# Performance work log

Hardware: AMD Instinct MI355X
Metric: run time of the kernel (lower is better)

The kernel has to match this reference:

```python
import jax, jax.numpy as jnp
import numpy as np

R = 32          # voxel resolution (init kwarg)
EPS = 0.0       # init kwarg eps


def _norm_coords(coords):
    # coords: [B, 3, N]
    nc = coords - coords.mean(axis=2, keepdims=True)
    # L2 norm over xyz (dim=1), max over points (dim=2)
    denom = jnp.linalg.norm(nc, axis=1, keepdims=True).max(axis=2, keepdims=True) * 2.0 + EPS
    nc = nc / denom + 0.5
    return jnp.clip(nc * R, 0.0, R - 1)  # [B, 3, N] in [0, R-1]


def setup_inputs() -> dict:
    key = jax.random.key(0)
    k1, k2 = jax.random.split(key)
    features = jax.random.normal(k1, (8, 64, 65536), dtype=jnp.float32)
    coords = jax.random.normal(k2, (8, 3, 65536), dtype=jnp.float32)
    return {"features": features, "coords": coords}


def reference(features, coords):
    # features: [B, C, N], coords: [B, 3, N]
    nc = _norm_coords(coords)
    vox = jnp.round(nc).astype(jnp.int32)                      # [B, 3, N]
    flat = (vox[:, 0] * R + vox[:, 1]) * R + vox[:, 2]         # [B, N] flat voxel ids

    def per_batch(f, idx):
        # f: [C, N], idx: [N] -> scatter-mean into R^3 voxels
        sums = jax.ops.segment_sum(f.T, idx, num_segments=R ** 3)            # [R^3, C]
        cnt = jax.ops.segment_sum(jnp.ones(idx.shape, jnp.float32), idx,
                                  num_segments=R ** 3)                        # [R^3]
        return (sums / jnp.maximum(cnt, 1.0)[:, None]).T                      # [C, R^3]

    vox_feat = jax.vmap(per_batch)(features, flat)             # [B, C, R^3]
    B, C = features.shape[0], features.shape[1]
    return vox_feat.reshape(B, C, R, R, R), nc
```

## Files before the change

kernel.cpp:

```cpp
#include <hip/hip_runtime.h>
#include <hip/hip_fp16.h>

#define RR 32
#define R3 32768
#define NPTS 65536
#define NCH 64
#define NB 8


__global__ void mean1_kernel(const float* __restrict__ coords, double* __restrict__ part) {
    __shared__ double ls[3][4];
    int b = blockIdx.y, blk = blockIdx.x;
    int t = threadIdx.x;
    const float* cb = coords + (size_t)b * 3 * NPTS;
    int base = blk * 1024 + t;
    double sx = 0.0, sy = 0.0, sz = 0.0;
#pragma unroll
    for (int k = 0; k < 4; k++) {
        int n = base + k * 256;
        sx += cb[n];
        sy += cb[NPTS + n];
        sz += cb[2 * NPTS + n];
    }
    for (int off = 32; off > 0; off >>= 1) {
        sx += __shfl_down(sx, off);
        sy += __shfl_down(sy, off);
        sz += __shfl_down(sz, off);
    }
    int wave = t >> 6;
    if ((t & 63) == 0) { ls[0][wave] = sx; ls[1][wave] = sy; ls[2][wave] = sz; }
    __syncthreads();
    if (t == 0) {
        part[((size_t)b * 64 + blk) * 3 + 0] = ls[0][0] + ls[0][1] + ls[0][2] + ls[0][3];
        part[((size_t)b * 64 + blk) * 3 + 1] = ls[1][0] + ls[1][1] + ls[1][2] + ls[1][3];
        part[((size_t)b * 64 + blk) * 3 + 2] = ls[2][0] + ls[2][1] + ls[2][2] + ls[2][3];
    }
}

__global__ void mean2_kernel(const double* __restrict__ part, float* __restrict__ meanf) {
    int b = blockIdx.x, l = threadIdx.x;
    double sx = part[((size_t)b * 64 + l) * 3 + 0];
    double sy = part[((size_t)b * 64 + l) * 3 + 1];
    double sz = part[((size_t)b * 64 + l) * 3 + 2];
    for (int off = 32; off > 0; off >>= 1) {
        sx += __shfl_down(sx, off);
        sy += __shfl_down(sy, off);
        sz += __shfl_down(sz, off);
    }
    if (l == 0) {
        meanf[b * 4 + 0] = (float)(sx * (1.0 / NPTS));
        meanf[b * 4 + 1] = (float)(sy * (1.0 / NPTS));
        meanf[b * 4 + 2] = (float)(sz * (1.0 / NPTS));
    }
}

__global__ void max1_kernel(const float* __restrict__ coords,
                            const float* __restrict__ meanf,
                            float* __restrict__ partmax) {
    __shared__ float ls[4];
    int b = blockIdx.y, blk = blockIdx.x;
    int t = threadIdx.x;
    float mx = meanf[b * 4 + 0], my = meanf[b * 4 + 1], mz = meanf[b * 4 + 2];
    const float* cb = coords + (size_t)b * 3 * NPTS;
    int base = blk * 1024 + t;
    float m = 0.0f;
#pragma unroll
    for (int k = 0; k < 4; k++) {
        int n = base + k * 256;
        float dx = cb[n] - mx;
        float dy = cb[NPTS + n] - my;
        float dz = cb[2 * NPTS + n] - mz;
        m = fmaxf(m, dx * dx + dy * dy + dz * dz);
    }
    for (int off = 32; off > 0; off >>= 1) m = fmaxf(m, __shfl_down(m, off));
    int wave = t >> 6;
    if ((t & 63) == 0) ls[wave] = m;
    __syncthreads();
    if (t == 0) partmax[b * 64 + blk] = fmaxf(fmaxf(ls[0], ls[1]), fmaxf(ls[2], ls[3]));
}

__global__ void max2_kernel(const float* __restrict__ partmax, float* __restrict__ denom) {
    int b = blockIdx.x, l = threadIdx.x;
    float m = partmax[b * 64 + l];
    for (int off = 32; off > 0; off >>= 1) m = fmaxf(m, __shfl_down(m, off));
    if (l == 0) denom[b] = 2.0f * sqrtf(m);
}


__global__ void nc_vid_kernel(const float* __restrict__ coords,
                              const float* __restrict__ meanf,
                              const float* __restrict__ denomv,
                              float* __restrict__ ncout,
                              int* __restrict__ vid,
                              unsigned* __restrict__ cnt) {
    int b = blockIdx.y;
    int n = blockIdx.x * blockDim.x + threadIdx.x;
    float mx = meanf[b * 4 + 0], my = meanf[b * 4 + 1], mz = meanf[b * 4 + 2];
    float denom = denomv[b];
    const float* cb = coords + (size_t)b * 3 * NPTS;
    float dx = cb[n] - mx;
    float dy = cb[NPTS + n] - my;
    float dz = cb[2 * NPTS + n] - mz;
    float qx = fminf(fmaxf((dx / denom + 0.5f) * 32.0f, 0.0f), 31.0f);
    float qy = fminf(fmaxf((dy / denom + 0.5f) * 32.0f, 0.0f), 31.0f);
    float qz = fminf(fmaxf((dz / denom + 0.5f) * 32.0f, 0.0f), 31.0f);
    float* nb_ = ncout + (size_t)b * 3 * NPTS;
    nb_[n] = qx;
    nb_[NPTS + n] = qy;
    nb_[2 * NPTS + n] = qz;
    int flat = ((int)rintf(qx) * RR + (int)rintf(qy)) * RR + (int)rintf(qz);
    vid[b * NPTS + n] = flat;
    atomicAdd(&cnt[b * R3 + flat], 1u);
}

__global__ __launch_bounds__(1024) void scan_kernel(const unsigned* __restrict__ cnt,
                                                    unsigned* __restrict__ cursor) {
    __shared__ unsigned buf[R3 + R3 / 32];
    __shared__ unsigned ls[1024];
    int b = blockIdx.x;
    int t = threadIdx.x;
    const unsigned* c = cnt + b * R3;
    for (int i = t; i < R3; i += 1024) buf[i + (i >> 5)] = c[i];
    __syncthreads();
    int sb = t * 33;
    unsigned v[32];
    unsigned s = 0;
#pragma unroll
    for (int k = 0; k < 32; k++) {
        unsigned x = buf[sb + k];
        v[k] = s;
        s += x;
    }
    ls[t] = s;
    __syncthreads();
    for (int d = 1; d < 1024; d <<= 1) {
        unsigned x = (t >= d) ? ls[t - d] : 0u;
        __syncthreads();
        ls[t] += x;
        __syncthreads();
    }
    unsigned chunk_excl = (t == 0) ? 0u : ls[t - 1];
#pragma unroll
    for (int k = 0; k < 32; k++) buf[sb + k] = chunk_excl + v[k];
    __syncthreads();
    unsigned* cur = cursor + b * R3;
    for (int i = t; i < R3; i += 1024) cur[i] = buf[i + (i >> 5)];
}

__global__ void permute_kernel(const float* __restrict__ feats,
                               const int* __restrict__ vid,
                               unsigned* __restrict__ cursor,
                               __half* __restrict__ ft,
                               int* __restrict__ vid_sorted) {
    __shared__ float tile[64][65];
    __shared__ int spos[64];
    int b  = blockIdx.y;
    int n0 = blockIdx.x * 64;
    int t  = threadIdx.x;

    if (t < 64) {
        int flat = vid[b * NPTS + n0 + t];
        int pos = (int)atomicAdd(&cursor[b * R3 + flat], 1u);
        spos[t] = pos;
        vid_sorted[b * NPTS + pos] = flat;
    }

    const float* fb = feats + (size_t)b * NCH * NPTS + n0;
    int i  = t & 63;
    int c0w = t >> 6;
#pragma unroll
    for (int iter = 0; iter < 16; iter++) {
        int c = iter * 4 + c0w;
        tile[i][c] = fb[(size_t)c * NPTS + i];
    }
    __syncthreads();

    int wave = t >> 6;
    int lane = t & 63;
    int hp = lane >> 5;
    int c0 = (lane & 31) * 2;
    __half* fbase = ft + (size_t)b * NPTS * NCH;
#pragma unroll
    for (int j = 0; j < 8; j++) {
        int p = wave * 16 + j * 2 + hp;
        __half2 hv = __floats2half2_rn(tile[p][c0], tile[p][c0 + 1]);
        *reinterpret_cast<__half2*>(fbase + (size_t)spos[p] * NCH + c0) = hv;
    }
}

__global__ void segsum_kernel(const __half* __restrict__ ft,
                              const int* __restrict__ vid_sorted,
                              float* __restrict__ ws_vox) {
    __shared__ int sv[257];
    int b   = blockIdx.y;
    int t   = threadIdx.x;
    int bp0 = blockIdx.x * 256;

    sv[t] = vid_sorted[b * NPTS + bp0 + t];
    if (t == 0)
        sv[256] = (bp0 + 256 < NPTS) ? vid_sorted[b * NPTS + bp0 + 256] : -1;
    __syncthreads();

    int wave  = t >> 6;
    int lane  = t & 63;
    int chunk = wave * 2 + (lane >> 5);
    int c0    = (lane & 31) * 2;
    int p0    = chunk * 32;

    const __half* fb = ft + ((size_t)b * NPTS + bp0 + p0) * NCH + c0;
    float* wv = ws_vox + (size_t)b * R3 * NCH + c0;

    float sx = 0.0f, sy = 0.0f;
    int vcur = sv[p0];
#pragma unroll
    for (int k = 0; k < 32; k++) {
        __half2 h = *reinterpret_cast<const __half2*>(fb + (size_t)k * NCH);
        float2 f = __half22float2(h);
        sx += f.x;
        sy += f.y;
        int vnext = sv[p0 + k + 1];
        if (vnext != vcur) {
            atomicAdd(wv + (size_t)vcur * NCH, sx);
            atomicAdd(wv + (size_t)vcur * NCH + 1, sy);
            sx = 0.0f;
            sy = 0.0f;
            vcur = vnext;
        }
    }
    if (sx != 0.0f || sy != 0.0f) {
        atomicAdd(wv + (size_t)vcur * NCH, sx);
        atomicAdd(wv + (size_t)vcur * NCH + 1, sy);
    }
}

__global__ void normalize_t_kernel(const float* __restrict__ ws_vox,
                                   const unsigned* __restrict__ cnt,
                                   float* __restrict__ voxout) {
    __shared__ float tile[64][65];
    __shared__ float cinv[64];
    __shared__ unsigned scnt[64];
    int b  = blockIdx.y;
    int v0 = blockIdx.x * 64;
    int t  = threadIdx.x;
    if (t < 64) {
        unsigned c = cnt[b * R3 + v0 + t];
        scnt[t] = c;
        cinv[t] = 1.0f / fmaxf((float)c, 1.0f);
    }
    __syncthreads();
    const float* src = ws_vox + ((size_t)b * R3 + v0) * NCH;
    int c = t & 63;
    int w = t >> 6;
#pragma unroll
    for (int iter = 0; iter < 16; iter++) {
        int vi = iter * 4 + w;
        tile[c][vi] = scnt[vi] ? src[(size_t)vi * NCH + c] * cinv[vi] : 0.0f;
    }
    __syncthreads();
    float* dst = voxout + (size_t)b * NCH * R3 + v0;
    int vi = t & 63;
#pragma unroll
    for (int iter = 0; iter < 16; iter++) {
        int cc = iter * 4 + w;
        dst[(size_t)cc * R3 + vi] = tile[cc][vi];
    }
}


__global__ void scatter_vm_kernel(const float* __restrict__ feats,
                                  const float* __restrict__ coords,
                                  const float* __restrict__ meanf,
                                  const float* __restrict__ denomv,
                                  float* __restrict__ ws_vox,
                                  float* __restrict__ ncout,
                                  float* __restrict__ cnt) {
    __shared__ float tile[64][65];
    __shared__ int   sflat[64];
    int b  = blockIdx.y;
    int n0 = blockIdx.x * 64;
    int t  = threadIdx.x;
    if (t < 64) {
        int n = n0 + t;
        float mx = meanf[b * 4 + 0], my = meanf[b * 4 + 1], mz = meanf[b * 4 + 2];
        float denom = denomv[b];
        const float* cb = coords + (size_t)b * 3 * NPTS;
        float dx = cb[n] - mx;
        float dy = cb[NPTS + n] - my;
        float dz = cb[2 * NPTS + n] - mz;
        float qx = fminf(fmaxf((dx / denom + 0.5f) * 32.0f, 0.0f), 31.0f);
        float qy = fminf(fmaxf((dy / denom + 0.5f) * 32.0f, 0.0f), 31.0f);
        float qz = fminf(fmaxf((dz / denom + 0.5f) * 32.0f, 0.0f), 31.0f);
        float* nb_ = ncout + (size_t)b * 3 * NPTS;
        nb_[n] = qx;
        nb_[NPTS + n] = qy;
        nb_[2 * NPTS + n] = qz;
        int flat = ((int)rintf(qx) * RR + (int)rintf(qy)) * RR + (int)rintf(qz);
        sflat[t] = flat;
        atomicAdd(&cnt[b * R3 + flat], 1.0f);
    }
    const float* fb = feats + (size_t)b * NCH * NPTS + n0;
    int i = t & 63;
    int c0 = t >> 6;
#pragma unroll
    for (int iter = 0; iter < 16; iter++) {
        int c = iter * 4 + c0;
        tile[i][c] = fb[(size_t)c * NPTS + i];
    }
    __syncthreads();
    int wave = t >> 6;
    int lane = t & 63;
#pragma unroll
    for (int k = 0; k < 16; k++) {
        int p = wave * 16 + k;
        float v = tile[p][lane];
        size_t base = ((size_t)b * R3 + sflat[p]) * NCH;
        atomicAdd(&ws_vox[base + lane], v);
    }
}

__global__ void normalize_tf_kernel(const float* __restrict__ ws_vox,
                                    const float* __restrict__ cnt,
                                    float* __restrict__ voxout) {
    __shared__ float tile[64][65];
    __shared__ float cinv[64];
    int b  = blockIdx.y;
    int v0 = blockIdx.x * 64;
    int t  = threadIdx.x;
    if (t < 64) cinv[t] = 1.0f / fmaxf(cnt[b * R3 + v0 + t], 1.0f);
    __syncthreads();
    const float* src = ws_vox + ((size_t)b * R3 + v0) * NCH;
    int c = t & 63;
    int w = t >> 6;
#pragma unroll
    for (int iter = 0; iter < 16; iter++) {
        int vi = iter * 4 + w;
        tile[c][vi] = src[(size_t)vi * NCH + c] * cinv[vi];
    }
    __syncthreads();
    float* dst = voxout + (size_t)b * NCH * R3 + v0;
    int vi = t & 63;
#pragma unroll
    for (int iter = 0; iter < 16; iter++) {
        int cc = iter * 4 + w;
        dst[(size_t)cc * R3 + vi] = tile[cc][vi];
    }
}

extern "C" void kernel_launch(void* const* d_in, const int* in_sizes, int n_in,
                              void* d_out, int out_size, void* d_ws, size_t ws_size,
                              hipStream_t stream) {
    const float* feats  = (const float*)d_in[0];
    const float* coords = (const float*)d_in[1];
    float* out = (float*)d_out;
    float* voxout = out;
    float* ncout  = out + (size_t)NB * NCH * R3;

    double* part    = (double*)d_ws;
    float*  partmax = (float*)((char*)d_ws + 12544);
    float*  meanf   = (float*)((char*)d_ws + 14592);
    float*  denomv  = (float*)((char*)d_ws + 14720);

    const size_t off_cnt   = 16384;
    const size_t cnt_bytes = (size_t)NB * R3 * 4;
    const size_t off_vox   = off_cnt + cnt_bytes;
    const size_t vox_bytes = (size_t)NB * R3 * NCH * 4;
    const size_t off_cur   = off_vox + vox_bytes;
    const size_t off_vid   = off_cur + cnt_bytes;
    const size_t vid_bytes = (size_t)NB * NPTS * 4;
    const size_t off_vs    = off_vid + vid_bytes;
    const size_t off_ft    = off_vs + vid_bytes;
    const size_t ft_bytes  = (size_t)NB * NPTS * NCH * 2;
    const size_t need_sort = off_ft + ft_bytes;
    const size_t need_vm   = off_vox + vox_bytes;

    if (ws_size >= need_sort) {
        unsigned* cnt    = (unsigned*)((char*)d_ws + off_cnt);
        float*    ws_vox = (float*)((char*)d_ws + off_vox);
        unsigned* cursor = (unsigned*)((char*)d_ws + off_cur);
        int*      vid    = (int*)((char*)d_ws + off_vid);
        int*      vid_s  = (int*)((char*)d_ws + off_vs);
        __half*   ft     = (__half*)((char*)d_ws + off_ft);

        hipMemsetAsync((char*)d_ws + off_cnt, 0, cnt_bytes + vox_bytes, stream);

        mean1_kernel<<<dim3(64, NB), 256, 0, stream>>>(coords, part);
        mean2_kernel<<<NB, 64, 0, stream>>>(part, meanf);
        max1_kernel <<<dim3(64, NB), 256, 0, stream>>>(coords, meanf, partmax);
        max2_kernel <<<NB, 64, 0, stream>>>(partmax, denomv);
        nc_vid_kernel<<<dim3(NPTS / 256, NB), 256, 0, stream>>>(coords, meanf, denomv,
                                                                ncout, vid, cnt);
        scan_kernel  <<<NB, 1024, 0, stream>>>(cnt, cursor);
        permute_kernel<<<dim3(NPTS / 64, NB), 256, 0, stream>>>(feats, vid, cursor, ft, vid_s);
        segsum_kernel <<<dim3(NPTS / 256, NB), 256, 0, stream>>>(ft, vid_s, ws_vox);
        normalize_t_kernel<<<dim3(R3 / 64, NB), 256, 0, stream>>>(ws_vox, cnt, voxout);
    } else if (ws_size >= need_vm) {
        float* cntf   = (float*)((char*)d_ws + off_cnt);
        float* ws_vox = (float*)((char*)d_ws + off_vox);
        hipMemsetAsync((char*)d_ws + off_cnt, 0, cnt_bytes + vox_bytes, stream);
        mean1_kernel<<<dim3(64, NB), 256, 0, stream>>>(coords, part);
        mean2_kernel<<<NB, 64, 0, stream>>>(part, meanf);
        max1_kernel <<<dim3(64, NB), 256, 0, stream>>>(coords, meanf, partmax);
        max2_kernel <<<NB, 64, 0, stream>>>(partmax, denomv);
        scatter_vm_kernel<<<dim3(NPTS / 64, NB), 256, 0, stream>>>(
            feats, coords, meanf, denomv, ws_vox, ncout, cntf);
        normalize_tf_kernel<<<dim3(R3 / 64, NB), 256, 0, stream>>>(ws_vox, cntf, voxout);
    }
}
```

Before: 342.7 us.

## Split permute into linear transpose plus rank kernel, gather features in segsum

Before, the permute kernel scattered fp16 feature rows to their sorted positions. Now the features are transposed into a point-major fp16 buffer with contiguous writes, and a separate rank kernel builds a permutation index. The segment-sum kernel then gathers rows through that permutation instead of reading them contiguously. This trades scattered 128-byte writes for scattered 128-byte reads and adds one kernel launch plus a perm buffer. The ws_size threshold for the fallback branch is also changed.

```diff
diff --git a/kernel.cpp b/kernel.cpp
--- a/kernel.cpp
+++ b/kernel.cpp
@@ -147,30 +147,19 @@
     for (int i = t; i < R3; i += 1024) cur[i] = buf[i + (i >> 5)];
 }
 
-__global__ void permute_kernel(const float* __restrict__ feats,
-                               const int* __restrict__ vid,
-                               unsigned* __restrict__ cursor,
-                               __half* __restrict__ ft,
-                               int* __restrict__ vid_sorted) {
+__global__ void transpose_kernel(const float* __restrict__ feats,
+                                 __half* __restrict__ ftL) {
     __shared__ float tile[64][65];
-    __shared__ int spos[64];
     int b  = blockIdx.y;
     int n0 = blockIdx.x * 64;
     int t  = threadIdx.x;
 
-    if (t < 64) {
-        int flat = vid[b * NPTS + n0 + t];
-        int pos = (int)atomicAdd(&cursor[b * R3 + flat], 1u);
-        spos[t] = pos;
-        vid_sorted[b * NPTS + pos] = flat;
-    }
-
     const float* fb = feats + (size_t)b * NCH * NPTS + n0;
     int i  = t & 63;
-    int c0w = t >> 6;
-#pragma unroll
-    for (int iter = 0; iter < 16; iter++) {
-        int c = iter * 4 + c0w;
+    int cw = t >> 6;
+#pragma unroll
+    for (int iter = 0; iter < 16; iter++) {
+        int c = iter * 4 + cw;
         tile[i][c] = fb[(size_t)c * NPTS + i];
     }
     __syncthreads();
@@ -179,24 +168,39 @@
     int lane = t & 63;
     int hp = lane >> 5;
     int c0 = (lane & 31) * 2;
-    __half* fbase = ft + (size_t)b * NPTS * NCH;
+    __half* fbase = ftL + ((size_t)b * NPTS + n0) * NCH;
 #pragma unroll
     for (int j = 0; j < 8; j++) {
         int p = wave * 16 + j * 2 + hp;
         __half2 hv = __floats2half2_rn(tile[p][c0], tile[p][c0 + 1]);
-        *reinterpret_cast<__half2*>(fbase + (size_t)spos[p] * NCH + c0) = hv;
-    }
-}
-
-__global__ void segsum_kernel(const __half* __restrict__ ft,
+        *reinterpret_cast<__half2*>(fbase + (size_t)p * NCH + c0) = hv;
+    }
+}
+
+__global__ void rank_kernel(const int* __restrict__ vid,
+                            unsigned* __restrict__ cursor,
+                            int* __restrict__ perm,
+                            int* __restrict__ vid_sorted) {
+    int b = blockIdx.y;
+    int n = blockIdx.x * blockDim.x + threadIdx.x;
+    int flat = vid[b * NPTS + n];
+    int pos = (int)atomicAdd(&cursor[b * R3 + flat], 1u);
+    perm[b * NPTS + pos] = n;
+    vid_sorted[b * NPTS + pos] = flat;
+}
+
+__global__ void segsum_kernel(const __half* __restrict__ ftL,
+                              const int* __restrict__ perm,
                               const int* __restrict__ vid_sorted,
                               float* __restrict__ ws_vox) {
     __shared__ int sv[257];
+    __shared__ int sp[256];
     int b   = blockIdx.y;
     int t   = threadIdx.x;
     int bp0 = blockIdx.x * 256;
 
     sv[t] = vid_sorted[b * NPTS + bp0 + t];
+    sp[t] = perm[b * NPTS + bp0 + t];
     if (t == 0)
         sv[256] = (bp0 + 256 < NPTS) ? vid_sorted[b * NPTS + bp0 + 256] : -1;
     __syncthreads();
@@ -207,14 +211,15 @@
     int c0    = (lane & 31) * 2;
     int p0    = chunk * 32;
 
-    const __half* fb = ft + ((size_t)b * NPTS + bp0 + p0) * NCH + c0;
+    const __half* fb = ftL + (size_t)b * NPTS * NCH + c0;
     float* wv = ws_vox + (size_t)b * R3 * NCH + c0;
 
     float sx = 0.0f, sy = 0.0f;
     int vcur = sv[p0];
 #pragma unroll
     for (int k = 0; k < 32; k++) {
-        __half2 h = *reinterpret_cast<const __half2*>(fb + (size_t)k * NCH);
+        int n = sp[p0 + k];
+        __half2 h = *reinterpret_cast<const __half2*>(fb + (size_t)n * NCH);
         float2 f = __half22float2(h);
         sx += f.x;
         sy += f.y;
@@ -368,10 +373,11 @@
     const size_t off_vid   = off_cur + cnt_bytes;
     const size_t vid_bytes = (size_t)NB * NPTS * 4;
     const size_t off_vs    = off_vid + vid_bytes;
-    const size_t off_ft    = off_vs + vid_bytes;
+    const size_t off_perm  = off_vs + vid_bytes;
+    const size_t off_ft    = off_perm + vid_bytes;
     const size_t ft_bytes  = (size_t)NB * NPTS * NCH * 2;
     const size_t need_sort = off_ft + ft_bytes;
-    const size_t need_vm   = off_vox + vox_bytes;
+    const size_t need_vm   = off_cur;
 
     if (ws_size >= need_sort) {
         unsigned* cnt    = (unsigned*)((char*)d_ws + off_cnt);
@@ -379,7 +385,8 @@
         unsigned* cursor = (unsigned*)((char*)d_ws + off_cur);
         int*      vid    = (int*)((char*)d_ws + off_vid);
         int*      vid_s  = (int*)((char*)d_ws + off_vs);
-        __half*   ft     = (__half*)((char*)d_ws + off_ft);
+        int*      perm   = (int*)((char*)d_ws + off_perm);
+        __half*   ftL    = (__half*)((char*)d_ws + off_ft);
 
         hipMemsetAsync((char*)d_ws + off_cnt, 0, cnt_bytes + vox_bytes, stream);
 
@@ -390,8 +397,9 @@
         nc_vid_kernel<<<dim3(NPTS / 256, NB), 256, 0, stream>>>(coords, meanf, denomv,
                                                                 ncout, vid, cnt);
         scan_kernel  <<<NB, 1024, 0, stream>>>(cnt, cursor);
-        permute_kernel<<<dim3(NPTS / 64, NB), 256, 0, stream>>>(feats, vid, cursor, ft, vid_s);
-        segsum_kernel <<<dim3(NPTS / 256, NB), 256, 0, stream>>>(ft, vid_s, ws_vox);
+        transpose_kernel<<<dim3(NPTS / 64, NB), 256, 0, stream>>>(feats, ftL);
+        rank_kernel  <<<dim3(NPTS / 256, NB), 256, 0, stream>>>(vid, cursor, perm, vid_s);
+        segsum_kernel<<<dim3(NPTS / 256, NB), 256, 0, stream>>>(ftL, perm, vid_s, ws_vox);
         normalize_t_kernel<<<dim3(R3 / 64, NB), 256, 0, stream>>>(ws_vox, cnt, voxout);
     } else if (ws_size >= need_vm) {
         float* cntf   = (float*)((char*)d_ws + off_cnt);
```

Measured after the change: 370.2 us. 1.08x slower.

## Fuse segment sum and normalize into per-voxel-tile shared-memory accumulation

Applied to the files above, without the earlier changes.

Replaces the point-parallel segment-sum kernel, which did global float atomics into a large voxel workspace, and the separate normalize/transpose kernel with one voxel-tile kernel. Each block owns 64 voxels, takes their point range from the scan cursors, accumulates sorted fp16 features in LDS with shared atomics, then normalizes and writes transposed output. This removes the 64 MB voxel workspace memset, the global atomics and the round trip through that buffer. The cost is uneven work per block when occupied voxels vary in point count, and the cursor semantics (inclusive end vs. start) must match how the scan and permute kernels use them.

```diff
diff --git a/kernel.cpp b/kernel.cpp
--- a/kernel.cpp
+++ b/kernel.cpp
@@ -1,5 +1,6 @@
 #include <hip/hip_runtime.h>
 #include <hip/hip_fp16.h>
+#include <climits>
 
 #define RR 32
 #define R3 32768
@@ -188,81 +189,83 @@
     }
 }
 
-__global__ void segsum_kernel(const __half* __restrict__ ft,
+__global__ void voxsum_kernel(const __half* __restrict__ ft,
                               const int* __restrict__ vid_sorted,
-                              float* __restrict__ ws_vox) {
+                              const unsigned* __restrict__ cursor,
+                              const unsigned* __restrict__ cnt,
+                              float* __restrict__ voxout) {
+    __shared__ float acc[64 * 65];
+    __shared__ float cinv[64];
     __shared__ int sv[257];
-    int b   = blockIdx.y;
-    int t   = threadIdx.x;
-    int bp0 = blockIdx.x * 256;
-
-    sv[t] = vid_sorted[b * NPTS + bp0 + t];
-    if (t == 0)
-        sv[256] = (bp0 + 256 < NPTS) ? vid_sorted[b * NPTS + bp0 + 256] : -1;
-    __syncthreads();
-
+    int b  = blockIdx.y;
+    int v0 = blockIdx.x * 64;
+    int t  = threadIdx.x;
+
+    for (int i = t; i < 64 * 65; i += 256) acc[i] = 0.0f;
+    if (t < 64) cinv[t] = 1.0f / fmaxf((float)cnt[b * R3 + v0 + t], 1.0f);
+
+    unsigned start = (v0 == 0) ? 0u : cursor[b * R3 + v0 - 1];
+    unsigned end   = cursor[b * R3 + v0 + 63];
+    __syncthreads();
+
+    const int* vs = vid_sorted + (size_t)b * NPTS;
     int wave  = t >> 6;
     int lane  = t & 63;
     int chunk = wave * 2 + (lane >> 5);
     int c0    = (lane & 31) * 2;
     int p0    = chunk * 32;
 
-    const __half* fb = ft + ((size_t)b * NPTS + bp0 + p0) * NCH + c0;
-    float* wv = ws_vox + (size_t)b * R3 * NCH + c0;
-
-    float sx = 0.0f, sy = 0.0f;
-    int vcur = sv[p0];
-#pragma unroll
-    for (int k = 0; k < 32; k++) {
-        __half2 h = *reinterpret_cast<const __half2*>(fb + (size_t)k * NCH);
-        float2 f = __half22float2(h);
-        sx += f.x;
-        sy += f.y;
-        int vnext = sv[p0 + k + 1];
-        if (vnext != vcur) {
-            atomicAdd(wv + (size_t)vcur * NCH, sx);
-            atomicAdd(wv + (size_t)vcur * NCH + 1, sy);
-            sx = 0.0f;
-            sy = 0.0f;
-            vcur = vnext;
+    for (unsigned tile0 = start; tile0 < end; tile0 += 256) {
+        unsigned p = tile0 + t;
+        sv[t] = (p < end) ? vs[p] : INT_MAX;
+        if (t == 0)
+            sv[256] = (tile0 + 256 < end) ? vs[tile0 + 256] : INT_MAX;
+        __syncthreads();
+
+        unsigned pg = tile0 + p0;
+        const __half* fb = ft + ((size_t)b * NPTS + pg) * NCH + c0;
+
+        float sx = 0.0f, sy = 0.0f;
+        int vcur = sv[p0];
+#pragma unroll
+        for (int k = 0; k < 32; k++) {
+            float fx = 0.0f, fy = 0.0f;
+            if (pg + k < end) {
+                __half2 h = *reinterpret_cast<const __half2*>(fb + (size_t)k * NCH);
+                float2 f = __half22float2(h);
+                fx = f.x; fy = f.y;
+            }
+            sx += fx;
+            sy += fy;
+            int vnext = sv[p0 + k + 1];
+            if (vnext != vcur) {
+                unsigned row = (unsigned)(vcur - v0);
+                if (row < 64u) {
+                    atomicAdd(&acc[row * 65 + c0], sx);
+                    atomicAdd(&acc[row * 65 + c0 + 1], sy);
+                }
+                sx = 0.0f;
+                sy = 0.0f;
+                vcur = vnext;
+            }
         }
-    }
-    if (sx != 0.0f || sy != 0.0f) {
-        atomicAdd(wv + (size_t)vcur * NCH, sx);
-        atomicAdd(wv + (size_t)vcur * NCH + 1, sy);
-    }
-}
-
-__global__ void normalize_t_kernel(const float* __restrict__ ws_vox,
-                                   const unsigned* __restrict__ cnt,
-                                   float* __restrict__ voxout) {
-    __shared__ float tile[64][65];
-    __shared__ float cinv[64];
-    __shared__ unsigned scnt[64];
-    int b  = blockIdx.y;
-    int v0 = blockIdx.x * 64;
-    int t  = threadIdx.x;
-    if (t < 64) {
-        unsigned c = cnt[b * R3 + v0 + t];
-        scnt[t] = c;
-        cinv[t] = 1.0f / fmaxf((float)c, 1.0f);
-    }
-    __syncthreads();
-    const float* src = ws_vox + ((size_t)b * R3 + v0) * NCH;
-    int c = t & 63;
-    int w = t >> 6;
-#pragma unroll
-    for (int iter = 0; iter < 16; iter++) {
-        int vi = iter * 4 + w;
-        tile[c][vi] = scnt[vi] ? src[(size_t)vi * NCH + c] * cinv[vi] : 0.0f;
-    }
-    __syncthreads();
+        if (sx != 0.0f || sy != 0.0f) {
+            unsigned row = (unsigned)(vcur - v0);
+            if (row < 64u) {
+                atomicAdd(&acc[row * 65 + c0], sx);
+                atomicAdd(&acc[row * 65 + c0 + 1], sy);
+            }
+        }
+        __syncthreads();
+    }
+
     float* dst = voxout + (size_t)b * NCH * R3 + v0;
-    int vi = t & 63;
-#pragma unroll
-    for (int iter = 0; iter < 16; iter++) {
-        int cc = iter * 4 + w;
-        dst[(size_t)cc * R3 + vi] = tile[cc][vi];
+    int qz = t & 63;
+    int cw = t >> 6;
+#pragma unroll
+    for (int it = 0; it < 16; it++) {
+        int c = it * 4 + cw;
+        dst[(size_t)c * R3 + qz] = acc[qz * 65 + c] * cinv[qz];
     }
 }
 
@@ -362,26 +365,26 @@
 
     const size_t off_cnt   = 16384;
     const size_t cnt_bytes = (size_t)NB * R3 * 4;
-    const size_t off_vox   = off_cnt + cnt_bytes;
-    const size_t vox_bytes = (size_t)NB * R3 * NCH * 4;
-    const size_t off_cur   = off_vox + vox_bytes;
+    const size_t off_cur   = off_cnt + cnt_bytes;
     const size_t off_vid   = off_cur + cnt_bytes;
     const size_t vid_bytes = (size_t)NB * NPTS * 4;
     const size_t off_vs    = off_vid + vid_bytes;
     const size_t off_ft    = off_vs + vid_bytes;
     const size_t ft_bytes  = (size_t)NB * NPTS * NCH * 2;
     const size_t need_sort = off_ft + ft_bytes;
+
+    const size_t off_vox   = off_cnt + cnt_bytes;
+    const size_t vox_bytes = (size_t)NB * R3 * NCH * 4;
     const size_t need_vm   = off_vox + vox_bytes;
 
     if (ws_size >= need_sort) {
         unsigned* cnt    = (unsigned*)((char*)d_ws + off_cnt);
-        float*    ws_vox = (float*)((char*)d_ws + off_vox);
         unsigned* cursor = (unsigned*)((char*)d_ws + off_cur);
         int*      vid    = (int*)((char*)d_ws + off_vid);
         int*      vid_s  = (int*)((char*)d_ws + off_vs);
         __half*   ft     = (__half*)((char*)d_ws + off_ft);
 
-        hipMemsetAsync((char*)d_ws + off_cnt, 0, cnt_bytes + vox_bytes, stream);
+        hipMemsetAsync((char*)d_ws + off_cnt, 0, cnt_bytes, stream);
 
         mean1_kernel<<<dim3(64, NB), 256, 0, stream>>>(coords, part);
         mean2_kernel<<<NB, 64, 0, stream>>>(part, meanf);
@@ -391,8 +394,7 @@
                                                                 ncout, vid, cnt);
         scan_kernel  <<<NB, 1024, 0, stream>>>(cnt, cursor);
         permute_kernel<<<dim3(NPTS / 64, NB), 256, 0, stream>>>(feats, vid, cursor, ft, vid_s);
-        segsum_kernel <<<dim3(NPTS / 256, NB), 256, 0, stream>>>(ft, vid_s, ws_vox);
-        normalize_t_kernel<<<dim3(R3 / 64, NB), 256, 0, stream>>>(ws_vox, cnt, voxout);
+        voxsum_kernel <<<dim3(R3 / 64, NB), 256, 0, stream>>>(ft, vid_s, cursor, cnt, voxout);
     } else if (ws_size >= need_vm) {
         float* cntf   = (float*)((char*)d_ws + off_cnt);
         float* ws_vox = (float*)((char*)d_ws + off_vox);
```

Result: slower. 457.4 us (+33.5%).

## Split per-batch voxel scan into multi-block three-pass scan; nontemporal permute stores

Applied to the files above, without the earlier changes.

Replaces the single-block-per-batch exclusive scan over 32768 voxel counts (8 blocks of 1024 threads) with a three-kernel scan. The first pass does 32 blocks per batch with uint4 loads, the second scans the block totals with wave shuffles, and the third adds the offsets back. This spreads the scan across far more CUs in exchange for two extra launches and an extra read/write of the cursor array. The permute kernel's scattered half2 stores to the sorted feature buffer also become nontemporal stores, to reduce cache pollution.

```diff
diff --git a/kernel.cpp b/kernel.cpp
--- a/kernel.cpp
+++ b/kernel.cpp
@@ -113,38 +113,52 @@
     atomicAdd(&cnt[b * R3 + flat], 1u);
 }
 
-__global__ __launch_bounds__(1024) void scan_kernel(const unsigned* __restrict__ cnt,
-                                                    unsigned* __restrict__ cursor) {
-    __shared__ unsigned buf[R3 + R3 / 32];
-    __shared__ unsigned ls[1024];
-    int b = blockIdx.x;
-    int t = threadIdx.x;
-    const unsigned* c = cnt + b * R3;
-    for (int i = t; i < R3; i += 1024) buf[i + (i >> 5)] = c[i];
-    __syncthreads();
-    int sb = t * 33;
-    unsigned v[32];
-    unsigned s = 0;
-#pragma unroll
-    for (int k = 0; k < 32; k++) {
-        unsigned x = buf[sb + k];
-        v[k] = s;
-        s += x;
-    }
+__global__ void scan1_kernel(const unsigned* __restrict__ cnt,
+                             unsigned* __restrict__ cursor,
+                             unsigned* __restrict__ tot) {
+    __shared__ unsigned ls[256];
+    int b = blockIdx.y, blk = blockIdx.x, t = threadIdx.x;
+    const unsigned* c = cnt + b * R3 + blk * 1024;
+    uint4 v = *reinterpret_cast<const uint4*>(c + t * 4);
+    unsigned s = v.x + v.y + v.z + v.w;
     ls[t] = s;
     __syncthreads();
-    for (int d = 1; d < 1024; d <<= 1) {
+    for (int d = 1; d < 256; d <<= 1) {
         unsigned x = (t >= d) ? ls[t - d] : 0u;
         __syncthreads();
         ls[t] += x;
         __syncthreads();
     }
-    unsigned chunk_excl = (t == 0) ? 0u : ls[t - 1];
-#pragma unroll
-    for (int k = 0; k < 32; k++) buf[sb + k] = chunk_excl + v[k];
-    __syncthreads();
-    unsigned* cur = cursor + b * R3;
-    for (int i = t; i < R3; i += 1024) cur[i] = buf[i + (i >> 5)];
+    unsigned base = (t == 0) ? 0u : ls[t - 1];
+    if (t == 255) tot[b * 32 + blk] = ls[255];
+    uint4 o;
+    o.x = base;
+    o.y = base + v.x;
+    o.z = base + v.x + v.y;
+    o.w = base + v.x + v.y + v.z;
+    *reinterpret_cast<uint4*>(cursor + b * R3 + blk * 1024 + t * 4) = o;
+}
+
+__global__ void scan2_kernel(unsigned* __restrict__ tot) {
+    int b = threadIdx.x >> 6;
+    int lane = threadIdx.x & 63;
+    unsigned v = (lane < 32) ? tot[b * 32 + lane] : 0u;
+    unsigned orig = v;
+    for (int d = 1; d < 32; d <<= 1) {
+        unsigned x = __shfl_up(v, d);
+        if (lane >= d && lane < 32) v += x;
+    }
+    if (lane < 32) tot[b * 32 + lane] = v - orig;
+}
+
+__global__ void scan3_kernel(unsigned* __restrict__ cursor,
+                             const unsigned* __restrict__ tot) {
+    int b = blockIdx.y, blk = blockIdx.x, t = threadIdx.x;
+    unsigned off = tot[b * 32 + blk];
+    uint4* p = reinterpret_cast<uint4*>(cursor + b * R3 + blk * 1024 + t * 4);
+    uint4 v = *p;
+    v.x += off; v.y += off; v.z += off; v.w += off;
+    *p = v;
 }
 
 __global__ void permute_kernel(const float* __restrict__ feats,
@@ -184,7 +198,9 @@
     for (int j = 0; j < 8; j++) {
         int p = wave * 16 + j * 2 + hp;
         __half2 hv = __floats2half2_rn(tile[p][c0], tile[p][c0 + 1]);
-        *reinterpret_cast<__half2*>(fbase + (size_t)spos[p] * NCH + c0) = hv;
+        unsigned u = *reinterpret_cast<unsigned*>(&hv);
+        __builtin_nontemporal_store(
+            u, reinterpret_cast<unsigned*>(fbase + (size_t)spos[p] * NCH + c0));
     }
 }
 
@@ -359,6 +375,7 @@
     float*  partmax = (float*)((char*)d_ws + 12544);
     float*  meanf   = (float*)((char*)d_ws + 14592);
     float*  denomv  = (float*)((char*)d_ws + 14720);
+    unsigned* tot   = (unsigned*)((char*)d_ws + 14848);
 
     const size_t off_cnt   = 16384;
     const size_t cnt_bytes = (size_t)NB * R3 * 4;
@@ -389,7 +406,9 @@
         max2_kernel <<<NB, 64, 0, stream>>>(partmax, denomv);
         nc_vid_kernel<<<dim3(NPTS / 256, NB), 256, 0, stream>>>(coords, meanf, denomv,
                                                                 ncout, vid, cnt);
-        scan_kernel  <<<NB, 1024, 0, stream>>>(cnt, cursor);
+        scan1_kernel<<<dim3(32, NB), 256, 0, stream>>>(cnt, cursor, tot);
+        scan2_kernel<<<1, 512, 0, stream>>>(tot);
+        scan3_kernel<<<dim3(32, NB), 256, 0, stream>>>(cursor, tot);
         permute_kernel<<<dim3(NPTS / 64, NB), 256, 0, stream>>>(feats, vid, cursor, ft, vid_s);
         segsum_kernel <<<dim3(NPTS / 256, NB), 256, 0, stream>>>(ft, vid_s, ws_vox);
         normalize_t_kernel<<<dim3(R3 / 64, NB), 256, 0, stream>>>(ws_vox, cnt, voxout);
```

Result: no change. 338.4 us (-1.2%).
